# Optimization experiments

Measured on AMD Instinct MI355X. Metric: run time of the kernel, lower is better.

The kernel has to match this reference:

```python
import jax, jax.numpy as jnp
from jax import lax
import numpy as np

EPS = 1e-3  # epsilon from __init__


def setup_inputs() -> dict:
    key = jax.random.key(0)
    k_x, k_m, k_v, k_p = jax.random.split(key, 4)
    B, C, H, W = 16, 64, 128, 128
    K = 8  # num_contexts
    x = jax.random.normal(k_x, (B, C, H, W), dtype=jnp.float32)
    # Parameters as initialized by reset_parameters():
    mean = jax.random.uniform(k_m, (K, 1), minval=-1.0, maxval=1.0, dtype=jnp.float32)
    variance = jax.random.uniform(k_v, (K, 1), minval=0.001, maxval=0.01, dtype=jnp.float32)
    p0 = jax.random.uniform(k_p, (K, 1), dtype=jnp.float32)
    prior = p0 / jnp.sum(p0, axis=0, keepdims=True)
    return {"x": x, "mean": mean, "variance": variance, "prior": prior}


def reference(x, mean, variance, prior):
    # Eval-mode forward of AdaptiveContextNorm (4D input path).
    mu = mean[:, 0]                      # (K,) scalar mean per context (expand over C is a broadcast)
    v = jax.nn.softplus(variance[:, 0])  # (K,)
    pr = jax.nn.softmax(prior[:, 0], axis=0)  # (K,)

    # Pass 1: mixture denominator. NOTE: faithful to source, the denominator
    # uses var WITHOUT +eps in the 4D path (ternary-precedence quirk), while
    # the numerator p_x_given_k uses (var + eps).
    def denom_step(acc, params):
        m, vv, pk = params
        return acc + pk * jnp.exp(-0.5 * ((x - m) / vv) ** 2), None

    denom, _ = lax.scan(denom_step, jnp.zeros_like(x), (mu, v, pr))

    # Pass 2: accumulate normalized output.
    def out_step(acc, params):
        m, vv, pk = params
        p_x_given_k = pk * jnp.exp(-0.5 * ((x - m) / (vv + EPS)) ** 2)
        tau_k = p_x_given_k / (denom + EPS)
        hat_x = (x - m) / jnp.sqrt(vv + EPS)
        return acc + tau_k / jnp.sqrt(pk + EPS) * hat_x, None

    out, _ = lax.scan(out_step, jnp.zeros_like(x), (mu, v, pr))
    return out
```

## Files before the change

### kernel.cpp

```cpp
#include <hip/hip_runtime.h>

#define ACN_EPS   0.001f
#define ACN_LOG2E 1.4426950408889634f

__global__ void acn_setup(const float* __restrict__ mean,
                          const float* __restrict__ variance,
                          const float* __restrict__ prior,
                          float* __restrict__ P) {
    int lane = threadIdx.x;
    int k = lane & 7;
    float m  = mean[k];
    float va = variance[k];
    float p0 = prior[k];

    float v = logf(1.0f + expf(va));
    float mx = p0;
    for (int off = 1; off < 8; off <<= 1) mx = fmaxf(mx, __shfl_xor(mx, off, 64));
    float e = expf(p0 - mx);
    float sum = e;
    for (int off = 1; off < 8; off <<= 1) sum += __shfl_xor(sum, off, 64);
    float pk = e / sum;

    float s1 = -0.5f * ACN_LOG2E / (v * v);
    float ve = v + ACN_EPS;
    float s2 = -0.5f * ACN_LOG2E / (ve * ve);
    float lp = log2f(pk);
    float lw = lp - 0.5f * log2f(pk + ACN_EPS) - 0.5f * log2f(ve);

    if (lane < 8) {
        P[k]      = m;
        P[8 + k]  = s1;
        P[16 + k] = s2;
        P[24 + k] = lp;
        P[32 + k] = lw;
    }
}

__device__ __forceinline__ float acn_elem(float x,
                                          const float* mu, const float* s1,
                                          const float* s2, const float* lp,
                                          const float* lw) {
    float denom = 0.0f, S = 0.0f;
#pragma unroll
    for (int k = 0; k < 8; ++k) {
        float d  = x - mu[k];
        float d2 = d * d;
        denom += __builtin_amdgcn_exp2f(fmaf(s1[k], d2, lp[k]));
        S = fmaf(__builtin_amdgcn_exp2f(fmaf(s2[k], d2, lw[k])), d, S);
    }
    return S * __builtin_amdgcn_rcpf(denom + ACN_EPS);
}

__global__ __launch_bounds__(256) void acn_main(const float4* __restrict__ x,
                                                float4* __restrict__ out,
                                                const float* __restrict__ P,
                                                int n4) {
    float mu[8], s1[8], s2[8], lp[8], lw[8];
#pragma unroll
    for (int k = 0; k < 8; ++k) {
        mu[k] = P[k];
        s1[k] = P[8 + k];
        s2[k] = P[16 + k];
        lp[k] = P[24 + k];
        lw[k] = P[32 + k];
    }

    int idx    = blockIdx.x * blockDim.x + threadIdx.x;
    int stride = gridDim.x * blockDim.x;
    for (int i = idx; i < n4; i += stride) {
        float4 xv = x[i];
        float4 ov;
        ov.x = acn_elem(xv.x, mu, s1, s2, lp, lw);
        ov.y = acn_elem(xv.y, mu, s1, s2, lp, lw);
        ov.z = acn_elem(xv.z, mu, s1, s2, lp, lw);
        ov.w = acn_elem(xv.w, mu, s1, s2, lp, lw);
        out[i] = ov;
    }
}

extern "C" void kernel_launch(void* const* d_in, const int* in_sizes, int n_in,
                              void* d_out, int out_size, void* d_ws, size_t ws_size,
                              hipStream_t stream) {
    const float* x        = (const float*)d_in[0];
    const float* mean     = (const float*)d_in[1];
    const float* variance = (const float*)d_in[2];
    const float* prior    = (const float*)d_in[3];
    float* out = (float*)d_out;
    float* P   = (float*)d_ws;

    acn_setup<<<1, 64, 0, stream>>>(mean, variance, prior, P);

    int n4 = out_size / 4;
    const int block = 256;
    const int grid  = 4096;
    acn_main<<<grid, block, 0, stream>>>((const float4*)x, (float4*)out, P, n4);
}
```

Baseline: 133.6 us.

## Replace second exponential with cubic Taylor correction of the first

The numerator exponential is rewritten as the denominator exponential times exp((s2-s1)*d^2). That correction factor is approximated by a cubic Taylor polynomial, with coefficients precomputed in the setup kernel. This swaps one transcendental per context and element for a few FMAs, aimed at relieving the transcendental-unit bottleneck. It also interleaves four elements per k, uses nontemporal stores and halves the grid. Accuracy depends on (s2-s1)*d^2 staying small, which holds because eps is small relative to the variance.

Result: faster. 129.1 us (-3.4%).

```diff
diff --git a/kernel.cpp b/kernel.cpp
--- a/kernel.cpp
+++ b/kernel.cpp
@@ -2,6 +2,9 @@
 
 #define ACN_EPS   0.001f
 #define ACN_LOG2E 1.4426950408889634f
+#define ACN_LN2   0.6931471805599453f
+
+typedef float v4f __attribute__((ext_vector_type(4)));
 
 __global__ void acn_setup(const float* __restrict__ mean,
                           const float* __restrict__ variance,
@@ -25,56 +28,64 @@
     float ve = v + ACN_EPS;
     float s2 = -0.5f * ACN_LOG2E / (ve * ve);
     float lp = log2f(pk);
-    float lw = lp - 0.5f * log2f(pk + ACN_EPS) - 0.5f * log2f(ve);
+    float C  = 1.0f / sqrtf((pk + ACN_EPS) * ve);
+    float ds = (s2 - s1) * ACN_LN2;
 
     if (lane < 8) {
         P[k]      = m;
         P[8 + k]  = s1;
-        P[16 + k] = s2;
-        P[24 + k] = lp;
-        P[32 + k] = lw;
+        P[16 + k] = lp;
+        P[24 + k] = ds;
+        P[32 + k] = C;
+        P[40 + k] = C * 0.5f;
+        P[48 + k] = C * (1.0f / 6.0f);
     }
 }
 
-__device__ __forceinline__ float acn_elem(float x,
-                                          const float* mu, const float* s1,
-                                          const float* s2, const float* lp,
-                                          const float* lw) {
-    float denom = 0.0f, S = 0.0f;
-#pragma unroll
-    for (int k = 0; k < 8; ++k) {
-        float d  = x - mu[k];
-        float d2 = d * d;
-        denom += __builtin_amdgcn_exp2f(fmaf(s1[k], d2, lp[k]));
-        S = fmaf(__builtin_amdgcn_exp2f(fmaf(s2[k], d2, lw[k])), d, S);
-    }
-    return S * __builtin_amdgcn_rcpf(denom + ACN_EPS);
-}
-
-__global__ __launch_bounds__(256) void acn_main(const float4* __restrict__ x,
-                                                float4* __restrict__ out,
+__global__ __launch_bounds__(256) void acn_main(const v4f* __restrict__ x,
+                                                v4f* __restrict__ out,
                                                 const float* __restrict__ P,
                                                 int n4) {
-    float mu[8], s1[8], s2[8], lp[8], lw[8];
+    float mu[8], s1[8], lp[8], ds[8], c0[8], c2[8], c3[8];
 #pragma unroll
     for (int k = 0; k < 8; ++k) {
         mu[k] = P[k];
         s1[k] = P[8 + k];
-        s2[k] = P[16 + k];
-        lp[k] = P[24 + k];
-        lw[k] = P[32 + k];
+        lp[k] = P[16 + k];
+        ds[k] = P[24 + k];
+        c0[k] = P[32 + k];
+        c2[k] = P[40 + k];
+        c3[k] = P[48 + k];
     }
 
     int idx    = blockIdx.x * blockDim.x + threadIdx.x;
     int stride = gridDim.x * blockDim.x;
     for (int i = idx; i < n4; i += stride) {
-        float4 xv = x[i];
-        float4 ov;
-        ov.x = acn_elem(xv.x, mu, s1, s2, lp, lw);
-        ov.y = acn_elem(xv.y, mu, s1, s2, lp, lw);
-        ov.z = acn_elem(xv.z, mu, s1, s2, lp, lw);
-        ov.w = acn_elem(xv.w, mu, s1, s2, lp, lw);
-        out[i] = ov;
+        v4f xv = x[i];
+        float xs[4]    = {xv.x, xv.y, xv.z, xv.w};
+        float denom[4] = {0.0f, 0.0f, 0.0f, 0.0f};
+        float S[4]     = {0.0f, 0.0f, 0.0f, 0.0f};
+#pragma unroll
+        for (int k = 0; k < 8; ++k) {
+#pragma unroll
+            for (int j = 0; j < 4; ++j) {
+                float d  = xs[j] - mu[k];
+                float d2 = d * d;
+                float E  = __builtin_amdgcn_exp2f(fmaf(s1[k], d2, lp[k]));
+                denom[j] += E;
+                float u  = ds[k] * d2;
+                float q  = fmaf(u, c3[k], c2[k]);
+                q        = fmaf(q, u, c0[k]);
+                q        = fmaf(q, u, c0[k]);
+                S[j]     = fmaf(E * d, q, S[j]);
+            }
+        }
+        v4f ov;
+        ov.x = S[0] * __builtin_amdgcn_rcpf(denom[0] + ACN_EPS);
+        ov.y = S[1] * __builtin_amdgcn_rcpf(denom[1] + ACN_EPS);
+        ov.z = S[2] * __builtin_amdgcn_rcpf(denom[2] + ACN_EPS);
+        ov.w = S[3] * __builtin_amdgcn_rcpf(denom[3] + ACN_EPS);
+        __builtin_nontemporal_store(ov, &out[i]);
     }
 }
 
@@ -92,6 +103,6 @@
 
     int n4 = out_size / 4;
     const int block = 256;
-    const int grid  = 4096;
-    acn_main<<<grid, block, 0, stream>>>((const float4*)x, (float4*)out, P, n4);
+    const int grid  = 2048;
+    acn_main<<<grid, block, 0, stream>>>((const v4f*)x, (v4f*)out, P, n4);
 }
```
